# Performance work log

Hardware: AMD Instinct MI355X
Metric: run time of the kernel (lower is better)

## Reference

```python
import jax, jax.numpy as jnp
import numpy as np

H = 10  # hidden size per direction
I = 1   # input size


def _lstm_scan(x_tbi, Wih, Whh, bih, bhh):
    """Single-direction LSTM over time-major input x_tbi: [T, B, I] -> [T, B, H].
    PyTorch gate order: i, f, g, o."""
    T, B, _ = x_tbi.shape
    # Precompute input contribution for all timesteps: [T, B, 4H]
    pre = jnp.einsum('tbi,gi->tbg', x_tbi, Wih) + bih + bhh

    def step(carry, p):
        h, c = carry
        gates = p + h @ Whh.T  # [B, 4H]
        i, f, g, o = jnp.split(gates, 4, axis=-1)
        i = jax.nn.sigmoid(i)
        f = jax.nn.sigmoid(f)
        g = jnp.tanh(g)
        o = jax.nn.sigmoid(o)
        c = f * c + i * g
        h = o * jnp.tanh(c)
        return (h, c), h

    h0 = jnp.zeros((B, H), x_tbi.dtype)
    (_, _), hs = jax.lax.scan(step, (h0, h0), pre)
    return hs  # [T, B, H]


def setup_inputs() -> dict:
    key = jax.random.key(0)
    ks = jax.random.split(key, 12)
    B, T = 256, 4096
    s = 1.0 / np.sqrt(H)  # PyTorch LSTM init range
    u = lambda k, shape: jax.random.uniform(k, shape, jnp.float32, -s, s)
    inp = {
        'data': jax.random.normal(ks[0], (B, T, I), jnp.float32),
        # forward direction
        'Wih_f': u(ks[1], (4 * H, I)),
        'Whh_f': u(ks[2], (4 * H, H)),
        'bih_f': u(ks[3], (4 * H,)),
        'bhh_f': u(ks[4], (4 * H,)),
        # backward direction
        'Wih_b': u(ks[5], (4 * H, I)),
        'Whh_b': u(ks[6], (4 * H, H)),
        'bih_b': u(ks[7], (4 * H,)),
        'bhh_b': u(ks[8], (4 * H,)),
        # final linear (kaiming_uniform fan_in=20 -> bound sqrt(6/20))
        'Wout': jax.random.uniform(ks[9], (1, 2 * H), jnp.float32, -np.sqrt(6.0 / (2 * H)), np.sqrt(6.0 / (2 * H))),
        'bout': jax.random.uniform(ks[10], (1,), jnp.float32, -1.0 / np.sqrt(2 * H), 1.0 / np.sqrt(2 * H)),
    }
    return inp


def reference(data, Wih_f, Whh_f, bih_f, bhh_f, Wih_b, Whh_b, bih_b, bhh_b, Wout, bout):
    # data: [B, T, 1] (batch_first) -> time-major [T, B, 1]
    x = jnp.transpose(data, (1, 0, 2))
    hf = _lstm_scan(x, Wih_f, Whh_f, bih_f, bhh_f)                 # [T, B, H]
    hb = _lstm_scan(x[::-1], Wih_b, Whh_b, bih_b, bhh_b)[::-1]     # [T, B, H]
    h = jnp.concatenate([hf, hb], axis=-1)                          # [T, B, 2H]
    y = h @ Wout.T + bout                                           # [T, B, 1]
    return jnp.transpose(y, (1, 0, 2))                              # [B, T, 1]
```

## Files before the change

### kernel.cpp

```cpp
#include <hip/hip_runtime.h>

#define T_LEN 4096
#define B_N   256
#define SEG_N 32
#define OWN   128
#define WARM  128
#define SMAX  (OWN + WARM)
#define YSTR  (SMAX + 2)
#define L2E   1.4426950408889634f

typedef float v2f __attribute__((ext_vector_type(2)));

__device__ __forceinline__ v2f pk_fma(v2f a, v2f b, v2f c) {
    v2f d; asm("v_pk_fma_f32 %0, %1, %2, %3" : "=v"(d) : "v"(a), "v"(b), "v"(c)); return d;
}

__global__ __launch_bounds__(64, 2) void Model_82008105550530_kernel(
    const float* __restrict__ data,
    const float* __restrict__ Wih_f, const float* __restrict__ Whh_f,
    const float* __restrict__ bih_f, const float* __restrict__ bhh_f,
    const float* __restrict__ Wih_b, const float* __restrict__ Whh_b,
    const float* __restrict__ bih_b, const float* __restrict__ bhh_b,
    const float* __restrict__ Wout, const float* __restrict__ bout,
    float* __restrict__ out)
{
    __shared__ __align__(16) v2f hbuf[144];
    __shared__ float ylds[8 * YSTR + 64];

    const int l = threadIdx.x;
    const int c = l >> 3;
    const int p = l & 7;

    const int bid = blockIdx.x;
    const int dir = bid >> 10;
    const int seg = (bid >> 5) & 31;
    const int b0  = (bid & 31) << 3;

    const float* Whh = dir ? Whh_b : Whh_f;
    const float* Wih = dir ? Wih_b : Wih_f;
    const float* bi  = dir ? bih_b : bih_f;
    const float* bh  = dir ? bhh_b : bhh_f;
    const float ybias = (dir == 0) ? bout[0] : 0.0f;

    v2f W2[4][10], wx2[4], bb2[4];
#pragma unroll
    for (int g = 0; g < 4; ++g) {
        wx2[g] = (v2f){0.f, 0.f}; bb2[g] = (v2f){0.f, 0.f};
#pragma unroll
        for (int m = 0; m < 10; ++m) W2[g][m] = (v2f){0.f, 0.f};
    }
    if (p < 5) {
#pragma unroll
        for (int g = 0; g < 4; ++g) {
            const float sc = (g == 2) ? (2.0f * L2E) : (-L2E);
            const int rA = g * 10 + 2 * p, rB = rA + 1;
#pragma unroll
            for (int m = 0; m < 10; ++m)
                W2[g][m] = (v2f){sc * Whh[rA * 10 + m], sc * Whh[rB * 10 + m]};
            wx2[g] = (v2f){sc * Wih[rA], sc * Wih[rB]};
            bb2[g] = (v2f){sc * (bi[rA] + bh[rA]), sc * (bi[rB] + bh[rB])};
        }
    } else if (p == 5) {
#pragma unroll
        for (int m = 0; m < 10; ++m) W2[0][m] = (v2f){Wout[dir * 10 + m], 0.f};
        bb2[0] = (v2f){ybias, 0.f};
    }

    const int hw1 = (p < 5) ? (c * 12 + 2 * p) : (96 + c * 6 + (p - 5) * 2);
    const int hw2 = hw1 + 1;
    int yw = (p == 5) ? (c * YSTR) : (8 * YSTR + l);
    const int ywd = (p == 5) ? 1 : 0;

    for (int i = l; i < 96; i += 64) hbuf[i] = (v2f){0.f, 0.f};

    const int wpre  = (dir == 0) ? ((seg == 0) ? 0 : WARM)
                                 : ((seg == SEG_N - 1) ? 0 : WARM);
    const int steps = OWN + wpre;

    const float* xrow = data + (size_t)(b0 + c) * T_LEN;
    const float* px = (dir == 0) ? (xrow + seg * OWN - wpre)
                                 : (xrow + seg * OWN + OWN - 1 + wpre - 7);
    const int pstep = (dir == 0) ? 8 : -8;
    float4 A  = *(const float4*)px;
    float4 Bv = *(const float4*)(px + 4);

    float Cx = 0.0f, Cy = 0.0f;
    const float4* hbF = (const float4*)&hbuf[c * 12];

#define UNIT_TAIL(GI, GF, GG, GO, CREG, HN)                                   \
    {                                                                         \
        const float qi = 1.0f + __builtin_amdgcn_exp2f(GI);                   \
        const float qf = 1.0f + __builtin_amdgcn_exp2f(GF);                   \
        const float qg = 1.0f + __builtin_amdgcn_exp2f(GG);                   \
        const float qo = 1.0f + __builtin_amdgcn_exp2f(GO);                   \
        const float p1 = qi * qf;                                             \
        const float p2 = p1 * qg;                                             \
        const float p3 = p2 * qo;                                             \
        const float R  = __builtin_amdgcn_rcpf(p3);                           \
        const float ro = p2 * R;                                              \
        const float R2 = qo * R;                                              \
        const float rg = p1 * R2;                                             \
        const float R1 = qg * R2;                                             \
        const float rf = qi * R1;                                             \
        const float ri = qf * R1;                                             \
        const float ai = (2.0f * L2E) * ri;                                   \
        const float ag = fmaf(-2.0f, rg, 1.0f);                               \
        CREG = fmaf(rf, CREG, ai * ag);                                       \
        const float r2 = __builtin_amdgcn_rcpf(                               \
            1.0f + __builtin_amdgcn_exp2f(CREG));                             \
        HN = fmaf(-2.0f * ro, r2, ro);                                        \
    }

#define STEP(XV)                                                              \
    {                                                                         \
        const v2f X2 = {XV, XV};                                              \
        v2f A0 = pk_fma(X2, wx2[0], bb2[0]);                                  \
        v2f A1 = pk_fma(X2, wx2[1], bb2[1]);                                  \
        v2f A2 = pk_fma(X2, wx2[2], bb2[2]);                                  \
        v2f A3 = pk_fma(X2, wx2[3], bb2[3]);                                  \
        const float4 P0 = hbF[0], P1 = hbF[1], P2 = hbF[2], P3 = hbF[3],      \
                     P4 = hbF[4];                                             \
        const v2f hp[10] = {{P0.x, P0.y}, {P0.z, P0.w}, {P1.x, P1.y},         \
                            {P1.z, P1.w}, {P2.x, P2.y}, {P2.z, P2.w},         \
                            {P3.x, P3.y}, {P3.z, P3.w}, {P4.x, P4.y},         \
                            {P4.z, P4.w}};                                    \
        _Pragma("unroll")                                                     \
        for (int m = 0; m < 10; ++m) {                                        \
            A0 = pk_fma(W2[0][m], hp[m], A0);                                 \
            A1 = pk_fma(W2[1][m], hp[m], A1);                                 \
            A2 = pk_fma(W2[2][m], hp[m], A2);                                 \
            A3 = pk_fma(W2[3][m], hp[m], A3);                                 \
        }                                                                     \
        ylds[yw] = A0.x;  yw += ywd;       \
        float hnx, hny;                                                       \
        UNIT_TAIL(A0.x, A1.x, A2.x, A3.x, Cx, hnx)                            \
        UNIT_TAIL(A0.y, A1.y, A2.y, A3.y, Cy, hny)                            \
        hbuf[hw1] = (v2f){hnx, hnx};                                          \
        hbuf[hw2] = (v2f){hny, hny};                                          \
    }

    const int nch = steps >> 3;
    for (int it = 0; it < nch; ++it) {
        const float* pn = px + ((it + 1 < nch) ? (it + 1) : it) * pstep;
        float4 An = *(const float4*)pn;
        float4 Bn = *(const float4*)(pn + 4);

        float q0 = A.x, q1 = A.y, q2 = A.z, q3 = A.w,
              q4 = Bv.x, q5 = Bv.y, q6 = Bv.z, q7 = Bv.w;
        if (dir) {
            float t;
            t = q0; q0 = q7; q7 = t;  t = q1; q1 = q6; q6 = t;
            t = q2; q2 = q5; q5 = t;  t = q3; q3 = q4; q4 = t;
        }
        STEP(q0) STEP(q1) STEP(q2) STEP(q3) STEP(q4) STEP(q5) STEP(q6) STEP(q7)
        A = An; Bv = Bn;
    }

    {
        v2f A0 = bb2[0];
        const float4 P0 = hbF[0], P1 = hbF[1], P2 = hbF[2], P3 = hbF[3],
                     P4 = hbF[4];
        const v2f hp[10] = {{P0.x, P0.y}, {P0.z, P0.w}, {P1.x, P1.y},
                            {P1.z, P1.w}, {P2.x, P2.y}, {P2.z, P2.w},
                            {P3.x, P3.y}, {P3.z, P3.w}, {P4.x, P4.y},
                            {P4.z, P4.w}};
#pragma unroll
        for (int m = 0; m < 10; ++m) A0 = pk_fma(W2[0][m], hp[m], A0);
        ylds[yw] = A0.x;
    }

    for (int i = l; i < 8 * OWN; i += 64) {
        const int ci = i >> 7;
        const int io = i & (OWN - 1);
        const int t  = seg * OWN + io;
        const int sp = (dir == 0) ? (wpre + io) : (OWN - 1 + wpre - io);
        atomicAdd(&out[(size_t)(b0 + ci) * T_LEN + t], ylds[ci * YSTR + sp + 1]);
    }
#undef STEP
#undef UNIT_TAIL
}

extern "C" void kernel_launch(void* const* d_in, const int* in_sizes, int n_in,
                              void* d_out, int out_size, void* d_ws, size_t ws_size,
                              hipStream_t stream) {
    const float* data  = (const float*)d_in[0];
    const float* Wih_f = (const float*)d_in[1];
    const float* Whh_f = (const float*)d_in[2];
    const float* bih_f = (const float*)d_in[3];
    const float* bhh_f = (const float*)d_in[4];
    const float* Wih_b = (const float*)d_in[5];
    const float* Whh_b = (const float*)d_in[6];
    const float* bih_b = (const float*)d_in[7];
    const float* bhh_b = (const float*)d_in[8];
    const float* Wout  = (const float*)d_in[9];
    const float* bout  = (const float*)d_in[10];
    float* out = (float*)d_out;

    hipMemsetAsync(out, 0, (size_t)out_size * sizeof(float), stream);
    Model_82008105550530_kernel<<<2048, 64, 0, stream>>>(
        data, Wih_f, Whh_f, bih_f, bhh_f, Wih_b, Whh_b, bih_b, bhh_b, Wout, bout, out);
}
```

Before: 134.5 us.

## Halve segment count, repack hidden-state layout, and use per-gate reciprocals

Segments double in length (16 segments of 256 owned steps), so the grid drops to 1024 blocks and the warm-up recomputation shrinks relative to owned work. Launch bounds go to one wave per SIMD. The hidden-state buffer becomes a compact float array: each lane keeps per-row weight pairs and reduces its dot products with packed FMAs plus a horizontal add. It writes one packed h pair per step instead of duplicated entries. The gate nonlinearity swaps the shared-reciprocal product trick for four separate reciprocals, which shortens the dependency chain at the cost of more transcendental ops. The longer serial chain per block and lower occupancy trade against less redundant warm-up work.

```diff
diff --git a/kernel.cpp b/kernel.cpp
--- a/kernel.cpp
+++ b/kernel.cpp
@@ -2,8 +2,8 @@
 
 #define T_LEN 4096
 #define B_N   256
-#define SEG_N 32
-#define OWN   128
+#define SEG_N 16
+#define OWN   256
 #define WARM  128
 #define SMAX  (OWN + WARM)
 #define YSTR  (SMAX + 2)
@@ -15,7 +15,7 @@
     v2f d; asm("v_pk_fma_f32 %0, %1, %2, %3" : "=v"(d) : "v"(a), "v"(b), "v"(c)); return d;
 }
 
-__global__ __launch_bounds__(64, 2) void Model_82008105550530_kernel(
+__global__ __launch_bounds__(64, 1) void Model_82008105550530_kernel(
     const float* __restrict__ data,
     const float* __restrict__ Wih_f, const float* __restrict__ Whh_f,
     const float* __restrict__ bih_f, const float* __restrict__ bhh_f,
@@ -24,7 +24,7 @@
     const float* __restrict__ Wout, const float* __restrict__ bout,
     float* __restrict__ out)
 {
-    __shared__ __align__(16) v2f hbuf[144];
+    __shared__ __align__(16) float hbuf[80 + 128];
     __shared__ float ylds[8 * YSTR + 64];
 
     const int l = threadIdx.x;
@@ -32,8 +32,8 @@
     const int p = l & 7;
 
     const int bid = blockIdx.x;
-    const int dir = bid >> 10;
-    const int seg = (bid >> 5) & 31;
+    const int dir = bid >> 9;
+    const int seg = (bid >> 5) & 15;
     const int b0  = (bid & 31) << 3;
 
     const float* Whh = dir ? Whh_b : Whh_f;
@@ -42,12 +42,13 @@
     const float* bh  = dir ? bhh_b : bhh_f;
     const float ybias = (dir == 0) ? bout[0] : 0.0f;
 
-    v2f W2[4][10], wx2[4], bb2[4];
+    v2f WA[4][5], WB[4][5];
+    float wxA[4], wxB[4], bA[4], bB[4];
 #pragma unroll
     for (int g = 0; g < 4; ++g) {
-        wx2[g] = (v2f){0.f, 0.f}; bb2[g] = (v2f){0.f, 0.f};
+        wxA[g] = wxB[g] = bA[g] = bB[g] = 0.f;
 #pragma unroll
-        for (int m = 0; m < 10; ++m) W2[g][m] = (v2f){0.f, 0.f};
+        for (int m = 0; m < 5; ++m) { WA[g][m] = (v2f){0.f, 0.f}; WB[g][m] = (v2f){0.f, 0.f}; }
     }
     if (p < 5) {
 #pragma unroll
@@ -55,23 +56,25 @@
             const float sc = (g == 2) ? (2.0f * L2E) : (-L2E);
             const int rA = g * 10 + 2 * p, rB = rA + 1;
 #pragma unroll
-            for (int m = 0; m < 10; ++m)
-                W2[g][m] = (v2f){sc * Whh[rA * 10 + m], sc * Whh[rB * 10 + m]};
-            wx2[g] = (v2f){sc * Wih[rA], sc * Wih[rB]};
-            bb2[g] = (v2f){sc * (bi[rA] + bh[rA]), sc * (bi[rB] + bh[rB])};
+            for (int m = 0; m < 5; ++m) {
+                WA[g][m] = (v2f){sc * Whh[rA * 10 + 2 * m], sc * Whh[rA * 10 + 2 * m + 1]};
+                WB[g][m] = (v2f){sc * Whh[rB * 10 + 2 * m], sc * Whh[rB * 10 + 2 * m + 1]};
+            }
+            wxA[g] = sc * Wih[rA];  wxB[g] = sc * Wih[rB];
+            bA[g]  = sc * (bi[rA] + bh[rA]);  bB[g] = sc * (bi[rB] + bh[rB]);
         }
     } else if (p == 5) {
 #pragma unroll
-        for (int m = 0; m < 10; ++m) W2[0][m] = (v2f){Wout[dir * 10 + m], 0.f};
-        bb2[0] = (v2f){ybias, 0.f};
+        for (int m = 0; m < 5; ++m)
+            WA[0][m] = (v2f){Wout[dir * 10 + 2 * m], Wout[dir * 10 + 2 * m + 1]};
+        bA[0] = ybias;
     }
 
-    const int hw1 = (p < 5) ? (c * 12 + 2 * p) : (96 + c * 6 + (p - 5) * 2);
-    const int hw2 = hw1 + 1;
+    const int hw = (p < 5) ? (c * 10 + 2 * p) : (80 + 2 * l);
     int yw = (p == 5) ? (c * YSTR) : (8 * YSTR + l);
     const int ywd = (p == 5) ? 1 : 0;
 
-    for (int i = l; i < 96; i += 64) hbuf[i] = (v2f){0.f, 0.f};
+    for (int i = l; i < 80; i += 64) hbuf[i] = 0.f;
 
     const int wpre  = (dir == 0) ? ((seg == 0) ? 0 : WARM)
                                  : ((seg == SEG_N - 1) ? 0 : WARM);
@@ -84,59 +87,51 @@
     float4 A  = *(const float4*)px;
     float4 Bv = *(const float4*)(px + 4);
 
-    float Cx = 0.0f, Cy = 0.0f;
-    const float4* hbF = (const float4*)&hbuf[c * 12];
+    float CA = 0.f, CB = 0.f;
+    const float* hrow = &hbuf[c * 10];
 
 #define UNIT_TAIL(GI, GF, GG, GO, CREG, HN)                                   \
     {                                                                         \
-        const float qi = 1.0f + __builtin_amdgcn_exp2f(GI);                   \
-        const float qf = 1.0f + __builtin_amdgcn_exp2f(GF);                   \
-        const float qg = 1.0f + __builtin_amdgcn_exp2f(GG);                   \
-        const float qo = 1.0f + __builtin_amdgcn_exp2f(GO);                   \
-        const float p1 = qi * qf;                                             \
-        const float p2 = p1 * qg;                                             \
-        const float p3 = p2 * qo;                                             \
-        const float R  = __builtin_amdgcn_rcpf(p3);                           \
-        const float ro = p2 * R;                                              \
-        const float R2 = qo * R;                                              \
-        const float rg = p1 * R2;                                             \
-        const float R1 = qg * R2;                                             \
-        const float rf = qi * R1;                                             \
-        const float ri = qf * R1;                                             \
-        const float ai = (2.0f * L2E) * ri;                                   \
-        const float ag = fmaf(-2.0f, rg, 1.0f);                               \
-        CREG = fmaf(rf, CREG, ai * ag);                                       \
+        const float ri = __builtin_amdgcn_rcpf(1.f + __builtin_amdgcn_exp2f(GI)); \
+        const float rf = __builtin_amdgcn_rcpf(1.f + __builtin_amdgcn_exp2f(GF)); \
+        const float rg = __builtin_amdgcn_rcpf(1.f + __builtin_amdgcn_exp2f(GG)); \
+        const float ro = __builtin_amdgcn_rcpf(1.f + __builtin_amdgcn_exp2f(GO)); \
+        const float ai = (2.f * L2E) * ri;                                    \
+        const float ag = fmaf(-2.f, rg, 1.f);                                 \
+        CREG = fmaf(rf, CREG, ai * ag);                     \
         const float r2 = __builtin_amdgcn_rcpf(                               \
-            1.0f + __builtin_amdgcn_exp2f(CREG));                             \
-        HN = fmaf(-2.0f * ro, r2, ro);                                        \
+            1.f + __builtin_amdgcn_exp2f(CREG));                              \
+        HN = fmaf(-2.f * ro, r2, ro);                      \
     }
 
 #define STEP(XV)                                                              \
     {                                                                         \
-        const v2f X2 = {XV, XV};                                              \
-        v2f A0 = pk_fma(X2, wx2[0], bb2[0]);                                  \
-        v2f A1 = pk_fma(X2, wx2[1], bb2[1]);                                  \
-        v2f A2 = pk_fma(X2, wx2[2], bb2[2]);                                  \
-        v2f A3 = pk_fma(X2, wx2[3], bb2[3]);                                  \
-        const float4 P0 = hbF[0], P1 = hbF[1], P2 = hbF[2], P3 = hbF[3],      \
-                     P4 = hbF[4];                                             \
-        const v2f hp[10] = {{P0.x, P0.y}, {P0.z, P0.w}, {P1.x, P1.y},         \
-                            {P1.z, P1.w}, {P2.x, P2.y}, {P2.z, P2.w},         \
-                            {P3.x, P3.y}, {P3.z, P3.w}, {P4.x, P4.y},         \
-                            {P4.z, P4.w}};                                    \
+        const float4 F0 = *(const float4*)&hrow[0];                           \
+        const float4 F1 = *(const float4*)&hrow[4];                           \
+        const v2f   H4 = *(const v2f*)&hrow[8];                               \
+        const v2f hp0 = {F0.x, F0.y}, hp1 = {F0.z, F0.w},                     \
+                  hp2 = {F1.x, F1.y}, hp3 = {F1.z, F1.w}, hp4 = H4;           \
+        float gA[4], gB[4];                                                   \
         _Pragma("unroll")                                                     \
-        for (int m = 0; m < 10; ++m) {                                        \
-            A0 = pk_fma(W2[0][m], hp[m], A0);                                 \
-            A1 = pk_fma(W2[1][m], hp[m], A1);                                 \
-            A2 = pk_fma(W2[2][m], hp[m], A2);                                 \
-            A3 = pk_fma(W2[3][m], hp[m], A3);                                 \
+        for (int g = 0; g < 4; ++g) {                                         \
+            v2f sA = pk_fma(WA[g][0], hp0, (v2f){fmaf(XV, wxA[g], bA[g]), 0.f}); \
+            sA = pk_fma(WA[g][1], hp1, sA);                                   \
+            sA = pk_fma(WA[g][2], hp2, sA);                                   \
+            sA = pk_fma(WA[g][3], hp3, sA);                                   \
+            sA = pk_fma(WA[g][4], hp4, sA);                                   \
+            gA[g] = sA.x + sA.y;                                              \
+            v2f sB = pk_fma(WB[g][0], hp0, (v2f){fmaf(XV, wxB[g], bB[g]), 0.f}); \
+            sB = pk_fma(WB[g][1], hp1, sB);                                   \
+            sB = pk_fma(WB[g][2], hp2, sB);                                   \
+            sB = pk_fma(WB[g][3], hp3, sB);                                   \
+            sB = pk_fma(WB[g][4], hp4, sB);                                   \
+            gB[g] = sB.x + sB.y;                                              \
         }                                                                     \
-        ylds[yw] = A0.x;  yw += ywd;       \
-        float hnx, hny;                                                       \
-        UNIT_TAIL(A0.x, A1.x, A2.x, A3.x, Cx, hnx)                            \
-        UNIT_TAIL(A0.y, A1.y, A2.y, A3.y, Cy, hny)                            \
-        hbuf[hw1] = (v2f){hnx, hnx};                                          \
-        hbuf[hw2] = (v2f){hny, hny};                                          \
+        ylds[yw] = gA[0];  yw += ywd;      \
+        float hnA, hnB;                                                       \
+        UNIT_TAIL(gA[0], gA[1], gA[2], gA[3], CA, hnA)                        \
+        UNIT_TAIL(gB[0], gB[1], gB[2], gB[3], CB, hnB)                        \
+        *(v2f*)&hbuf[hw] = (v2f){hnA, hnB};          \
     }
 
     const int nch = steps >> 3;
@@ -157,20 +152,21 @@
     }
 
     {
-        v2f A0 = bb2[0];
-        const float4 P0 = hbF[0], P1 = hbF[1], P2 = hbF[2], P3 = hbF[3],
-                     P4 = hbF[4];
-        const v2f hp[10] = {{P0.x, P0.y}, {P0.z, P0.w}, {P1.x, P1.y},
-                            {P1.z, P1.w}, {P2.x, P2.y}, {P2.z, P2.w},
-                            {P3.x, P3.y}, {P3.z, P3.w}, {P4.x, P4.y},
-                            {P4.z, P4.w}};
-#pragma unroll
-        for (int m = 0; m < 10; ++m) A0 = pk_fma(W2[0][m], hp[m], A0);
-        ylds[yw] = A0.x;
+        const float4 F0 = *(const float4*)&hrow[0];
+        const float4 F1 = *(const float4*)&hrow[4];
+        const v2f   H4 = *(const v2f*)&hrow[8];
+        const v2f hp0 = {F0.x, F0.y}, hp1 = {F0.z, F0.w},
+                  hp2 = {F1.x, F1.y}, hp3 = {F1.z, F1.w}, hp4 = H4;
+        v2f sA = pk_fma(WA[0][0], hp0, (v2f){bA[0], 0.f});
+        sA = pk_fma(WA[0][1], hp1, sA);
+        sA = pk_fma(WA[0][2], hp2, sA);
+        sA = pk_fma(WA[0][3], hp3, sA);
+        sA = pk_fma(WA[0][4], hp4, sA);
+        ylds[yw] = sA.x + sA.y;
     }
 
     for (int i = l; i < 8 * OWN; i += 64) {
-        const int ci = i >> 7;
+        const int ci = i >> 8;
         const int io = i & (OWN - 1);
         const int t  = seg * OWN + io;
         const int sp = (dir == 0) ? (wpre + io) : (OWN - 1 + wpre - io);
@@ -197,6 +193,6 @@
     float* out = (float*)d_out;
 
     hipMemsetAsync(out, 0, (size_t)out_size * sizeof(float), stream);
-    Model_82008105550530_kernel<<<2048, 64, 0, stream>>>(
+    Model_82008105550530_kernel<<<1024, 64, 0, stream>>>(
         data, Wih_f, Whh_f, bih_f, bhh_f, Wih_b, Whh_b, bih_b, bhh_b, Wout, bout, out);
 }
```

Result: slower. 166.2 us (+23.6%).
